# Kernel optimization log

Measured on AMD Instinct MI355X. Metric: run time of the kernel, lower is better.

The kernel has to match this reference:

```python
import math
import jax, jax.numpy as jnp
import numpy as np

BLOCK = 256
LAYER_IDX = 5
NUM_HIDDEN_LAYERS = 32


def get_slopes(head_dim):
    equ = lambda x: 1 / 2 ** (8 / x)
    log2 = math.log2(head_dim)
    if log2.is_integer():
        return [equ(head_dim) ** i for i in range(1, head_dim + 1)]
    lower = 2 ** math.floor(log2)
    upper = 2 ** math.ceil(log2)
    ls = get_slopes(lower)
    us = get_slopes(upper)
    return ls + us[::2][: head_dim - lower]


def setup_inputs() -> dict:
    key = jax.random.key(0)
    k1, k2, k3 = jax.random.split(key, 3)
    B, H, S, D = 2, 64, 4096, 64
    q = jax.random.normal(k1, (B, H, S, D), dtype=jnp.float32)
    k = jax.random.normal(k2, (B, H, S, D), dtype=jnp.float32)
    v = jax.random.normal(k3, (B, H, S, D), dtype=jnp.float32)
    mask = jnp.ones((B, S), dtype=jnp.int32)
    return {"query_states": q, "key_states": k, "value_states": v, "attention_mask": mask}


def _lightning_attention(q, k, v, attention_mask):
    B, H, S, D = q.shape
    E = v.shape[-1]
    # mask padded positions in values
    v = v * attention_mask[:, None, :, None].astype(v.dtype)

    # per-head decay slopes, scaled by layer depth (note: H == D by construction)
    slopes = np.asarray(get_slopes(D), dtype=np.float32)
    slopes = slopes * (1.0 - LAYER_IDX / (NUM_HIDDEN_LAYERS - 1) + 1e-05)
    slope = jnp.asarray(slopes)[:, None, None]  # [H, 1, 1]

    arr = jnp.arange(1, BLOCK + 1, dtype=jnp.float32)
    q_decay = jnp.exp(-slope * arr[:, None])            # [H, BLOCK, 1]
    k_decay = jnp.exp(-slope * (BLOCK - arr)[:, None])  # [H, BLOCK, 1]
    idx = arr[:, None] - arr[None, :]                   # [BLOCK, BLOCK]
    s_idx = slope * idx[None]                           # [H, BLOCK, BLOCK] (slope [H,1,1] broadcasts)
    diag_decay = jnp.exp(jnp.where(idx[None] >= 0, -s_idx, -jnp.inf))  # [H, BLOCK, BLOCK]
    block_decay = jnp.exp(-slope * BLOCK)               # [H, 1, 1]

    nb = S // BLOCK
    qb = q.reshape(B, H, nb, BLOCK, D).transpose(2, 0, 1, 3, 4)  # [nb, B, H, BLOCK, D]
    kb = k.reshape(B, H, nb, BLOCK, D).transpose(2, 0, 1, 3, 4)
    vb = v.reshape(B, H, nb, BLOCK, E).transpose(2, 0, 1, 3, 4)

    def step(kv, blk):
        qi, ki, vi = blk  # each [B, H, BLOCK, D/E]
        # inter-block: decayed query reads recurrent kv state
        o_inter = jnp.einsum('bhmd,bhde->bhme', qi * q_decay, kv)
        # intra-block: causal decayed attention within the block
        qk = jnp.einsum('bhmd,bhnd->bhmn', qi, ki) * diag_decay
        o_intra = jnp.einsum('bhmn,bhne->bhme', qk, vi)
        # update recurrent state
        kv_new = block_decay * kv + jnp.einsum('bhmd,bhme->bhde', ki * k_decay, vi)
        return kv_new, o_inter + o_intra

    kv0 = jnp.zeros((B, H, D, E), dtype=jnp.float32)
    _, outs = jax.lax.scan(step, kv0, (qb, kb, vb))  # outs: [nb, B, H, BLOCK, E]
    out = outs.transpose(1, 2, 0, 3, 4).reshape(B, H, S, E)
    return out


def reference(query_states, key_states, value_states, attention_mask):
    return _lightning_attention(query_states, key_states, value_states, attention_mask)
```

## Files before the change

### kernel.cpp

```cpp
#include <hip/hip_runtime.h>

typedef __attribute__((ext_vector_type(4))) float f4;
typedef __attribute__((ext_vector_type(4))) float f32x4;
typedef __attribute__((ext_vector_type(8))) short short8;
typedef __attribute__((ext_vector_type(4))) short short4v;

#define S_  4096
#define NB_ 16
#define SLOPE_SCALE 0.838719677419355f

__device__ __forceinline__ float slope_for_head(int h) {
    return exp2f(-(float)(h + 1) * 0.125f) * SLOPE_SCALE;
}

__device__ __forceinline__ short f2bf(float f) {
    unsigned u = __float_as_uint(f);
    u += 0x7FFFu + ((u >> 16) & 1u);
    return (short)(u >> 16);
}
__device__ __forceinline__ float bf2f(short s) {
    return __uint_as_float(((unsigned)(unsigned short)s) << 16);
}

template<int USE_KBF>
__global__ __launch_bounds__(256, 2) void phase1_kvblocks(
    const float* __restrict__ k, const float* __restrict__ v,
    const int* __restrict__ mask, float* __restrict__ kvt,
    short* __restrict__ vt, short* __restrict__ kbf)
{
    __shared__ float ks[64][64];
    __shared__ float vs[64][64];
    __shared__ short khi[64][72];
    __shared__ short klo[64][72];
    __shared__ short vhi[64][72];
    __shared__ short vlo[64][72];
    const int j  = blockIdx.x;
    const int bh = blockIdx.y;
    const int b  = bh >> 6;
    const int h  = bh & 63;
    const int t  = threadIdx.x;
    const int wave = t >> 6, lane = t & 63, quad = lane >> 4, l16 = lane & 15;
    const float slope = slope_for_head(h);

    const f32x4 zf = {0.f, 0.f, 0.f, 0.f};
    f32x4 acc[4];
    acc[0] = zf; acc[1] = zf; acc[2] = zf; acc[3] = zf;

    const long long tilebase = ((long long)bh * S_ + j * 256) * 64;
    const long long vtbase   = ((long long)(bh * NB_ + j)) * 16384;

    for (int c = 0; c < 4; ++c) {
        for (int i = 0; i < 4; ++i) {
            int fi  = t + i * 256;
            int row = fi >> 4;
            int col = (fi & 15) << 2;
            long long g = tilebase + (long long)(c * 64 + row) * 64 + col;
            f4 kk = *(const f4*)(k + g);
            if (USE_KBF) {
                short4v kb = { f2bf(kk.x), f2bf(kk.y), f2bf(kk.z), f2bf(kk.w) };
                *(short4v*)(kbf + g) = kb;
            }
            float kd = __expf(-slope * (float)(255 - (c * 64 + row)));
            *(f4*)&ks[row][col] = kk * kd;
            f4 vv = *(const f4*)(v + g);
            float mv = (float)mask[b * S_ + j * 256 + c * 64 + row];
            *(f4*)&vs[row][col] = vv * mv;
        }
        __syncthreads();

        {
            const int dl = lane;
            #pragma unroll
            for (int r = 0; r < 16; r += 8) {
                short8 k8h, k8l, v8h, v8l;
                #pragma unroll
                for (int rr = 0; rr < 8; ++rr) {
                    int n = wave * 16 + r + rr;
                    float kx = ks[n][dl];
                    short kh = f2bf(kx);
                    k8h[rr] = kh; k8l[rr] = f2bf(kx - bf2f(kh));
                    float vx = vs[n][dl];
                    short vh = f2bf(vx);
                    v8h[rr] = vh; v8l[rr] = f2bf(vx - bf2f(vh));
                }
                *(short8*)&khi[dl][wave * 16 + r] = k8h;
                *(short8*)&klo[dl][wave * 16 + r] = k8l;
                *(short8*)&vhi[dl][wave * 16 + r] = v8h;
                *(short8*)&vlo[dl][wave * 16 + r] = v8l;
            }
        }
        __syncthreads();

        {
            int e  = t >> 2;
            int nb = (t & 3) << 4;
            short8 w0 = *(const short8*)&vhi[e][nb];
            short8 w1 = *(const short8*)&vhi[e][nb + 8];
            long long g = vtbase + (long long)(c * 2 + (nb >> 5)) * 2048
                        + e * 32 + (nb & 31);
            *(short8*)(vt + g)     = w0;
            *(short8*)(vt + g + 8) = w1;
        }

        #pragma unroll
        for (int cc = 0; cc < 2; ++cc) {
            const int nb = cc * 32 + quad * 8;
            short8 ahi = *(const short8*)&vhi[wave * 16 + l16][nb];
            short8 alo = *(const short8*)&vlo[wave * 16 + l16][nb];
            #pragma unroll
            for (int dt = 0; dt < 4; ++dt) {
                short8 bhi = *(const short8*)&khi[dt * 16 + l16][nb];
                short8 blo = *(const short8*)&klo[dt * 16 + l16][nb];
                acc[dt] = __builtin_amdgcn_mfma_f32_16x16x32_bf16(ahi, bhi, acc[dt], 0, 0, 0);
                acc[dt] = __builtin_amdgcn_mfma_f32_16x16x32_bf16(ahi, blo, acc[dt], 0, 0, 0);
                acc[dt] = __builtin_amdgcn_mfma_f32_16x16x32_bf16(alo, bhi, acc[dt], 0, 0, 0);
            }
        }
        __syncthreads();
    }

    float* o = kvt + ((long long)(bh * NB_ + j)) * 4096;
    #pragma unroll
    for (int dt = 0; dt < 4; ++dt) {
        #pragma unroll
        for (int r = 0; r < 4; ++r) {
            int e = wave * 16 + quad * 4 + r;
            o[e * 64 + dt * 16 + l16] = acc[dt][r];
        }
    }
}

__global__ __launch_bounds__(256) void phase2_scan(float* __restrict__ kvt)
{
    const int g    = blockIdx.x;
    const int bh   = g >> 2;
    const int part = g & 3;
    const int h    = bh & 63;
    const float slope = slope_for_head(h);
    const float bd = __expf(-slope * 256.0f);

    f4* base = (f4*)(kvt + (long long)bh * NB_ * 4096) + part * 256 + threadIdx.x;
    f4 vals[NB_];
    #pragma unroll
    for (int jj = 0; jj < NB_; ++jj) vals[jj] = base[jj * 1024];
    f4 st = {0.f, 0.f, 0.f, 0.f};
    #pragma unroll
    for (int jj = 0; jj < NB_; ++jj) {
        base[jj * 1024] = st;
        st = st * bd + vals[jj];
    }
}

template<int USE_KBF>
__global__ __launch_bounds__(256, 2) void phase3_output(
    const float* __restrict__ q, const float* __restrict__ kfp,
    const short* __restrict__ kbf, const float* __restrict__ kvt,
    const short* __restrict__ vt, float* __restrict__ out)
{
    __shared__ short P[4][64 * 56];
    const int j    = blockIdx.x;
    const int bh   = blockIdx.y;
    const int h    = bh & 63;
    const int tid  = threadIdx.x;
    const int wave = tid >> 6;
    const int lane = tid & 63;
    const int quad = lane >> 4;
    const int l16  = lane & 15;
    const int wrole  = (wave + j) & 3;
    const float slope = slope_for_head(h);
    const int mwbase = wrole << 6;

    const long long rowbase = (long long)bh * S_ + j * 256 + mwbase;

    short8 qf[4][2];
    #pragma unroll
    for (int mt = 0; mt < 4; ++mt) {
        const float* qp = q + (rowbase + mt * 16 + l16) * 64 + quad * 8;
        #pragma unroll
        for (int ks = 0; ks < 2; ++ks) {
            f4 a = *(const f4*)(qp + ks * 32);
            f4 b = *(const f4*)(qp + ks * 32 + 4);
            short8 f;
            f[0] = f2bf(a.x); f[1] = f2bf(a.y); f[2] = f2bf(a.z); f[3] = f2bf(a.w);
            f[4] = f2bf(b.x); f[5] = f2bf(b.y); f[6] = f2bf(b.z); f[7] = f2bf(b.w);
            qf[mt][ks] = f;
        }
    }

    const f32x4 zf = {0.f, 0.f, 0.f, 0.f};
    f32x4 of[4][4];
    #pragma unroll
    for (int et = 0; et < 4; ++et)
        #pragma unroll
        for (int mt = 0; mt < 4; ++mt) of[et][mt] = zf;

    const float* kvp = kvt + ((long long)(bh * NB_ + j) << 12);
    #pragma unroll
    for (int et = 0; et < 4; ++et) {
        #pragma unroll
        for (int ks = 0; ks < 2; ++ks) {
            const float* p = kvp + (et * 16 + l16) * 64 + ks * 32 + quad * 8;
            f4 a = *(const f4*)(p);
            f4 b = *(const f4*)(p + 4);
            short8 af;
            af[0] = f2bf(a.x); af[1] = f2bf(a.y); af[2] = f2bf(a.z); af[3] = f2bf(a.w);
            af[4] = f2bf(b.x); af[5] = f2bf(b.y); af[6] = f2bf(b.z); af[7] = f2bf(b.w);
            #pragma unroll
            for (int mt = 0; mt < 4; ++mt)
                of[et][mt] = __builtin_amdgcn_mfma_f32_16x16x32_bf16(
                    af, qf[mt][ks], of[et][mt], 0, 0, 0);
        }
    }
    #pragma unroll
    for (int mt = 0; mt < 4; ++mt) {
        float qd = __expf(-slope * (float)(mwbase + mt * 16 + l16 + 1));
        #pragma unroll
        for (int et = 0; et < 4; ++et) of[et][mt] *= qd;
    }

    const float er1 = __expf(slope);
    const float er2 = er1 * er1;
    const float er3 = er2 * er1;
    short* Pw = &P[wave][0];
    const int nchunks = (mwbase >> 5) + 2;
    const long long kTile = ((long long)bh * S_ + j * 256) * 64;
    const long long vTile = ((long long)(bh * NB_ + j)) * 16384;

    for (int c = 0; c < nchunks; ++c) {
        const int nbase = c << 5;

        short8 kf[2][2];
        if (USE_KBF) {
            #pragma unroll
            for (int nt = 0; nt < 2; ++nt) {
                const short* kp = kbf + kTile
                    + (long long)(nbase + nt * 16 + l16) * 64 + quad * 8;
                kf[nt][0] = *(const short8*)(kp);
                kf[nt][1] = *(const short8*)(kp + 32);
            }
        } else {
            #pragma unroll
            for (int nt = 0; nt < 2; ++nt) {
                const float* kp = kfp + kTile
                    + (long long)(nbase + nt * 16 + l16) * 64 + quad * 8;
                #pragma unroll
                for (int ks = 0; ks < 2; ++ks) {
                    f4 a = *(const f4*)(kp + ks * 32);
                    f4 b = *(const f4*)(kp + ks * 32 + 4);
                    short8 f;
                    f[0] = f2bf(a.x); f[1] = f2bf(a.y); f[2] = f2bf(a.z); f[3] = f2bf(a.w);
                    f[4] = f2bf(b.x); f[5] = f2bf(b.y); f[6] = f2bf(b.z); f[7] = f2bf(b.w);
                    kf[nt][ks] = f;
                }
            }
        }

        f32x4 sf[2][4];
        #pragma unroll
        for (int nt = 0; nt < 2; ++nt)
            #pragma unroll
            for (int mt = 0; mt < 4; ++mt) sf[nt][mt] = zf;
        #pragma unroll
        for (int nt = 0; nt < 2; ++nt)
            #pragma unroll
            for (int ks = 0; ks < 2; ++ks)
                #pragma unroll
                for (int mt = 0; mt < 4; ++mt)
                    sf[nt][mt] = __builtin_amdgcn_mfma_f32_16x16x32_bf16(
                        kf[nt][ks], qf[mt][ks], sf[nt][mt], 0, 0, 0);

        #pragma unroll
        for (int nt = 0; nt < 2; ++nt) {
            #pragma unroll
            for (int mt = 0; mt < 4; ++mt) {
                int n0 = nbase + nt * 16 + quad * 4;
                int m  = mwbase + mt * 16 + l16;
                float ddb = __expf(-slope * (float)(m - n0));
                f32x4 s = sf[nt][mt];
                float v0 = (m >= n0)     ? s[0] * ddb       : 0.f;
                float v1 = (m >= n0 + 1) ? s[1] * ddb * er1 : 0.f;
                float v2 = (m >= n0 + 2) ? s[2] * ddb * er2 : 0.f;
                float v3 = (m >= n0 + 3) ? s[3] * ddb * er3 : 0.f;
                short4v pk = {f2bf(v0), f2bf(v1), f2bf(v2), f2bf(v3)};
                *(short4v*)&Pw[(mt * 16 + l16) * 56 + nt * 16 + quad * 4] = pk;
            }
        }
        asm volatile("s_waitcnt lgkmcnt(0)" ::: "memory");

        short8 pb[4];
        #pragma unroll
        for (int mt = 0; mt < 4; ++mt)
            pb[mt] = *(const short8*)&Pw[(mt * 16 + l16) * 56 + quad * 8];
        short8 va[4];
        #pragma unroll
        for (int et = 0; et < 4; ++et)
            va[et] = *(const short8*)(vt + vTile + c * 2048
                                      + (et * 16 + l16) * 32 + quad * 8);

        #pragma unroll
        for (int et = 0; et < 4; ++et)
            #pragma unroll
            for (int mt = 0; mt < 4; ++mt)
                of[et][mt] = __builtin_amdgcn_mfma_f32_16x16x32_bf16(
                    va[et], pb[mt], of[et][mt], 0, 0, 0);
    }

    #pragma unroll
    for (int mt = 0; mt < 4; ++mt) {
        float* orow = out + (rowbase + mt * 16 + l16) * 64;
        #pragma unroll
        for (int et = 0; et < 4; ++et) {
            f4 o = {of[et][mt][0], of[et][mt][1], of[et][mt][2], of[et][mt][3]};
            *(f4*)(orow + et * 16 + quad * 4) = o;
        }
    }
}

extern "C" void kernel_launch(void* const* d_in, const int* in_sizes, int n_in,
                              void* d_out, int out_size, void* d_ws, size_t ws_size,
                              hipStream_t stream) {
    const float* q    = (const float*)d_in[0];
    const float* k    = (const float*)d_in[1];
    const float* v    = (const float*)d_in[2];
    const int*   mask = (const int*)d_in[3];
    float* kvt = (float*)d_ws;
    short* vt  = (short*)((char*)d_ws + (size_t)33554432);
    short* kbf = (short*)((char*)d_ws + (size_t)33554432 + 67108864);
    float* out = (float*)d_out;

    const bool use_kbf = ws_size >= (size_t)167772160;
    if (use_kbf) {
        phase1_kvblocks<1><<<dim3(16, 128), 256, 0, stream>>>(k, v, mask, kvt, vt, kbf);
        phase2_scan<<<512, 256, 0, stream>>>(kvt);
        phase3_output<1><<<dim3(16, 128), 256, 0, stream>>>(q, k, kbf, kvt, vt, out);
    } else {
        phase1_kvblocks<0><<<dim3(16, 128), 256, 0, stream>>>(k, v, mask, kvt, vt, kbf);
        phase2_scan<<<512, 256, 0, stream>>>(kvt);
        phase3_output<0><<<dim3(16, 128), 256, 0, stream>>>(q, k, kbf, kvt, vt, out);
    }
}
```

Before: 518.3 us.

## Pipeline K/V staging, swizzle LDS, emit bf16 KV state, prefetch K chunks

Phase 1 now works in 32-row sub-tiles with register prefetch of the next K/V sub-tile, a smaller XOR-swizzled LDS layout, and higher occupancy bounds. Phase 2 can also write a bf16 copy of the scanned KV state, so phase 3 loads packed bf16 instead of converting fp32. Phase 3 double-buffers the bf16 K fragments across chunks, issues the V loads earlier, and replaces the per-element exp with precomputed decay factors. The bf16 state path only runs if the workspace is large enough, and the extra register buffers may add register pressure.

Measured after the change: 496.2 us. 4.3% less time.

```diff
diff --git a/kernel.cpp b/kernel.cpp
--- a/kernel.cpp
+++ b/kernel.cpp
@@ -22,18 +22,22 @@
     return __uint_as_float(((unsigned)(unsigned short)s) << 16);
 }
 
+__device__ __forceinline__ int NX(int row, int n8) {
+    return n8 ^ (((row >> 3) & 3) << 3);
+}
+
 template<int USE_KBF>
-__global__ __launch_bounds__(256, 2) void phase1_kvblocks(
+__global__ __launch_bounds__(256, 4) void phase1_kvblocks(
     const float* __restrict__ k, const float* __restrict__ v,
     const int* __restrict__ mask, float* __restrict__ kvt,
     short* __restrict__ vt, short* __restrict__ kbf)
 {
-    __shared__ float ks[64][64];
-    __shared__ float vs[64][64];
-    __shared__ short khi[64][72];
-    __shared__ short klo[64][72];
-    __shared__ short vhi[64][72];
-    __shared__ short vlo[64][72];
+    __shared__ float ks[32][64];
+    __shared__ float vs[32][64];
+    __shared__ short khi[64][40];
+    __shared__ short klo[64][40];
+    __shared__ short vhi[64][40];
+    __shared__ short vlo[64][40];
     const int j  = blockIdx.x;
     const int bh = blockIdx.y;
     const int b  = bh >> 6;
@@ -49,68 +53,77 @@
     const long long tilebase = ((long long)bh * S_ + j * 256) * 64;
     const long long vtbase   = ((long long)(bh * NB_ + j)) * 16384;
 
-    for (int c = 0; c < 4; ++c) {
-        for (int i = 0; i < 4; ++i) {
-            int fi  = t + i * 256;
-            int row = fi >> 4;
-            int col = (fi & 15) << 2;
-            long long g = tilebase + (long long)(c * 64 + row) * 64 + col;
-            f4 kk = *(const f4*)(k + g);
+    const int r0  = t >> 4;
+    const int col = (t & 15) << 2;
+
+    f4 kr0, kr1, vr0, vr1; int mr0, mr1;
+    auto LOADSTG = [&](int ss) {
+        long long g0 = tilebase + (long long)(ss * 32 + r0) * 64 + col;
+        kr0 = *(const f4*)(k + g0);
+        vr0 = *(const f4*)(v + g0);
+        kr1 = *(const f4*)(k + g0 + 16 * 64);
+        vr1 = *(const f4*)(v + g0 + 16 * 64);
+        mr0 = mask[b * S_ + j * 256 + ss * 32 + r0];
+        mr1 = mask[b * S_ + j * 256 + ss * 32 + r0 + 16];
+    };
+    LOADSTG(0);
+
+    for (int ss = 0; ss < 8; ++ss) {
+        {
+            int gn0 = ss * 32 + r0;
             if (USE_KBF) {
-                short4v kb = { f2bf(kk.x), f2bf(kk.y), f2bf(kk.z), f2bf(kk.w) };
-                *(short4v*)(kbf + g) = kb;
-            }
-            float kd = __expf(-slope * (float)(255 - (c * 64 + row)));
-            *(f4*)&ks[row][col] = kk * kd;
-            f4 vv = *(const f4*)(v + g);
-            float mv = (float)mask[b * S_ + j * 256 + c * 64 + row];
-            *(f4*)&vs[row][col] = vv * mv;
-        }
+                long long g0 = tilebase + (long long)gn0 * 64 + col;
+                short4v kb0 = { f2bf(kr0.x), f2bf(kr0.y), f2bf(kr0.z), f2bf(kr0.w) };
+                short4v kb1 = { f2bf(kr1.x), f2bf(kr1.y), f2bf(kr1.z), f2bf(kr1.w) };
+                *(short4v*)(kbf + g0)           = kb0;
+                *(short4v*)(kbf + g0 + 16 * 64) = kb1;
+            }
+            float kd0 = __expf(-slope * (float)(255 - gn0));
+            float kd1 = __expf(-slope * (float)(255 - gn0 - 16));
+            *(f4*)&ks[r0][col]      = kr0 * kd0;
+            *(f4*)&ks[r0 + 16][col] = kr1 * kd1;
+            *(f4*)&vs[r0][col]      = vr0 * (float)mr0;
+            *(f4*)&vs[r0 + 16][col] = vr1 * (float)mr1;
+        }
+        if (ss < 7) LOADSTG(ss + 1);
         __syncthreads();
 
         {
             const int dl = lane;
-            #pragma unroll
-            for (int r = 0; r < 16; r += 8) {
-                short8 k8h, k8l, v8h, v8l;
-                #pragma unroll
-                for (int rr = 0; rr < 8; ++rr) {
-                    int n = wave * 16 + r + rr;
-                    float kx = ks[n][dl];
-                    short kh = f2bf(kx);
-                    k8h[rr] = kh; k8l[rr] = f2bf(kx - bf2f(kh));
-                    float vx = vs[n][dl];
-                    short vh = f2bf(vx);
-                    v8h[rr] = vh; v8l[rr] = f2bf(vx - bf2f(vh));
-                }
-                *(short8*)&khi[dl][wave * 16 + r] = k8h;
-                *(short8*)&klo[dl][wave * 16 + r] = k8l;
-                *(short8*)&vhi[dl][wave * 16 + r] = v8h;
-                *(short8*)&vlo[dl][wave * 16 + r] = v8l;
-            }
+            short8 k8h, k8l, v8h, v8l;
+            #pragma unroll
+            for (int rr = 0; rr < 8; ++rr) {
+                float kx = ks[wave * 8 + rr][dl];
+                short kh = f2bf(kx);
+                k8h[rr] = kh; k8l[rr] = f2bf(kx - bf2f(kh));
+                float vx = vs[wave * 8 + rr][dl];
+                short vh = f2bf(vx);
+                v8h[rr] = vh; v8l[rr] = f2bf(vx - bf2f(vh));
+            }
+            int ni = NX(dl, wave * 8);
+            *(short8*)&khi[dl][ni] = k8h;
+            *(short8*)&klo[dl][ni] = k8l;
+            *(short8*)&vhi[dl][ni] = v8h;
+            *(short8*)&vlo[dl][ni] = v8l;
         }
         __syncthreads();
 
         {
             int e  = t >> 2;
-            int nb = (t & 3) << 4;
-            short8 w0 = *(const short8*)&vhi[e][nb];
-            short8 w1 = *(const short8*)&vhi[e][nb + 8];
-            long long g = vtbase + (long long)(c * 2 + (nb >> 5)) * 2048
-                        + e * 32 + (nb & 31);
-            *(short8*)(vt + g)     = w0;
-            *(short8*)(vt + g + 8) = w1;
-        }
-
-        #pragma unroll
-        for (int cc = 0; cc < 2; ++cc) {
-            const int nb = cc * 32 + quad * 8;
-            short8 ahi = *(const short8*)&vhi[wave * 16 + l16][nb];
-            short8 alo = *(const short8*)&vlo[wave * 16 + l16][nb];
+            int nb = (t & 3) << 3;
+            short8 w = *(const short8*)&vhi[e][NX(e, nb)];
+            *(short8*)(vt + vtbase + ss * 2048 + e * 32 + nb) = w;
+        }
+
+        {
+            int ar = wave * 16 + l16;
+            short8 ahi = *(const short8*)&vhi[ar][NX(ar, quad * 8)];
+            short8 alo = *(const short8*)&vlo[ar][NX(ar, quad * 8)];
             #pragma unroll
             for (int dt = 0; dt < 4; ++dt) {
-                short8 bhi = *(const short8*)&khi[dt * 16 + l16][nb];
-                short8 blo = *(const short8*)&klo[dt * 16 + l16][nb];
+                int br = dt * 16 + l16;
+                short8 bhi = *(const short8*)&khi[br][NX(br, quad * 8)];
+                short8 blo = *(const short8*)&klo[br][NX(br, quad * 8)];
                 acc[dt] = __builtin_amdgcn_mfma_f32_16x16x32_bf16(ahi, bhi, acc[dt], 0, 0, 0);
                 acc[dt] = __builtin_amdgcn_mfma_f32_16x16x32_bf16(ahi, blo, acc[dt], 0, 0, 0);
                 acc[dt] = __builtin_amdgcn_mfma_f32_16x16x32_bf16(alo, bhi, acc[dt], 0, 0, 0);
@@ -130,7 +143,9 @@
     }
 }
 
-__global__ __launch_bounds__(256) void phase2_scan(float* __restrict__ kvt)
+template<int EMIT>
+__global__ __launch_bounds__(256) void phase2_scan(float* __restrict__ kvt,
+                                                   short* __restrict__ kvb)
 {
     const int g    = blockIdx.x;
     const int bh   = g >> 2;
@@ -140,6 +155,8 @@
     const float bd = __expf(-slope * 256.0f);
 
     f4* base = (f4*)(kvt + (long long)bh * NB_ * 4096) + part * 256 + threadIdx.x;
+    short* kb = kvb + (long long)bh * NB_ * 4096
+              + ((long long)(part * 256 + threadIdx.x) << 2);
     f4 vals[NB_];
     #pragma unroll
     for (int jj = 0; jj < NB_; ++jj) vals[jj] = base[jj * 1024];
@@ -147,15 +164,20 @@
     #pragma unroll
     for (int jj = 0; jj < NB_; ++jj) {
         base[jj * 1024] = st;
+        if (EMIT) {
+            short4v sb = { f2bf(st.x), f2bf(st.y), f2bf(st.z), f2bf(st.w) };
+            *(short4v*)(kb + (long long)jj * 4096) = sb;
+        }
         st = st * bd + vals[jj];
     }
 }
 
-template<int USE_KBF>
-__global__ __launch_bounds__(256, 2) void phase3_output(
+template<int USE_KBF, int USE_KVB>
+__global__ __launch_bounds__(256, 3) void phase3_output(
     const float* __restrict__ q, const float* __restrict__ kfp,
     const short* __restrict__ kbf, const float* __restrict__ kvt,
-    const short* __restrict__ vt, float* __restrict__ out)
+    const short* __restrict__ kvb, const short* __restrict__ vt,
+    float* __restrict__ out)
 {
     __shared__ short P[4][64 * 56];
     const int j    = blockIdx.x;
@@ -171,6 +193,8 @@
     const int mwbase = wrole << 6;
 
     const long long rowbase = (long long)bh * S_ + j * 256 + mwbase;
+    const long long kTile = ((long long)bh * S_ + j * 256) * 64;
+    const long long vTile = ((long long)(bh * NB_ + j)) * 16384;
 
     short8 qf[4][2];
     #pragma unroll
@@ -187,6 +211,19 @@
         }
     }
 
+    auto LOADKF = [&](short8 (&dst)[2][2], int nb0) {
+        #pragma unroll
+        for (int nt = 0; nt < 2; ++nt) {
+            const short* kp = kbf + kTile
+                + (long long)(nb0 + nt * 16 + l16) * 64 + quad * 8;
+            dst[nt][0] = *(const short8*)(kp);
+            dst[nt][1] = *(const short8*)(kp + 32);
+        }
+    };
+
+    short8 kfA[2][2];
+    if (USE_KBF) LOADKF(kfA, 0);
+
     const f32x4 zf = {0.f, 0.f, 0.f, 0.f};
     f32x4 of[4][4];
     #pragma unroll
@@ -194,21 +231,37 @@
         #pragma unroll
         for (int mt = 0; mt < 4; ++mt) of[et][mt] = zf;
 
-    const float* kvp = kvt + ((long long)(bh * NB_ + j) << 12);
-    #pragma unroll
-    for (int et = 0; et < 4; ++et) {
-        #pragma unroll
-        for (int ks = 0; ks < 2; ++ks) {
-            const float* p = kvp + (et * 16 + l16) * 64 + ks * 32 + quad * 8;
-            f4 a = *(const f4*)(p);
-            f4 b = *(const f4*)(p + 4);
-            short8 af;
-            af[0] = f2bf(a.x); af[1] = f2bf(a.y); af[2] = f2bf(a.z); af[3] = f2bf(a.w);
-            af[4] = f2bf(b.x); af[5] = f2bf(b.y); af[6] = f2bf(b.z); af[7] = f2bf(b.w);
-            #pragma unroll
-            for (int mt = 0; mt < 4; ++mt)
-                of[et][mt] = __builtin_amdgcn_mfma_f32_16x16x32_bf16(
-                    af, qf[mt][ks], of[et][mt], 0, 0, 0);
+    if (USE_KVB) {
+        const short* kvbp = kvb + ((long long)(bh * NB_ + j) << 12);
+        #pragma unroll
+        for (int et = 0; et < 4; ++et) {
+            #pragma unroll
+            for (int ks = 0; ks < 2; ++ks) {
+                short8 af = *(const short8*)(kvbp + (et * 16 + l16) * 64
+                                             + ks * 32 + quad * 8);
+                #pragma unroll
+                for (int mt = 0; mt < 4; ++mt)
+                    of[et][mt] = __builtin_amdgcn_mfma_f32_16x16x32_bf16(
+                        af, qf[mt][ks], of[et][mt], 0, 0, 0);
+            }
+        }
+    } else {
+        const float* kvp = kvt + ((long long)(bh * NB_ + j) << 12);
+        #pragma unroll
+        for (int et = 0; et < 4; ++et) {
+            #pragma unroll
+            for (int ks = 0; ks < 2; ++ks) {
+                const float* p = kvp + (et * 16 + l16) * 64 + ks * 32 + quad * 8;
+                f4 a = *(const f4*)(p);
+                f4 b = *(const f4*)(p + 4);
+                short8 af;
+                af[0] = f2bf(a.x); af[1] = f2bf(a.y); af[2] = f2bf(a.z); af[3] = f2bf(a.w);
+                af[4] = f2bf(b.x); af[5] = f2bf(b.y); af[6] = f2bf(b.z); af[7] = f2bf(b.w);
+                #pragma unroll
+                for (int mt = 0; mt < 4; ++mt)
+                    of[et][mt] = __builtin_amdgcn_mfma_f32_16x16x32_bf16(
+                        af, qf[mt][ks], of[et][mt], 0, 0, 0);
+            }
         }
     }
     #pragma unroll
@@ -221,24 +274,28 @@
     const float er1 = __expf(slope);
     const float er2 = er1 * er1;
     const float er3 = er2 * er1;
+    const float L  = __expf(-slope * (float)(l16 - quad * 4));
+    const float T1 = __expf(-slope * 16.f);
+    const float Ti = __expf(slope * 16.f);
+    const float Tm[4] = {1.f, T1, T1 * T1, T1 * T1 * T1};
+
     short* Pw = &P[wave][0];
     const int nchunks = (mwbase >> 5) + 2;
-    const long long kTile = ((long long)bh * S_ + j * 256) * 64;
-    const long long vTile = ((long long)(bh * NB_ + j)) * 16384;
 
     for (int c = 0; c < nchunks; ++c) {
         const int nbase = c << 5;
-
-        short8 kf[2][2];
-        if (USE_KBF) {
-            #pragma unroll
-            for (int nt = 0; nt < 2; ++nt) {
-                const short* kp = kbf + kTile
-                    + (long long)(nbase + nt * 16 + l16) * 64 + quad * 8;
-                kf[nt][0] = *(const short8*)(kp);
-                kf[nt][1] = *(const short8*)(kp + 32);
-            }
-        } else {
+        const bool havenext = (c + 1 < nchunks);
+
+        short8 va[4];
+        #pragma unroll
+        for (int et = 0; et < 4; ++et)
+            va[et] = *(const short8*)(vt + vTile + c * 2048
+                                      + (et * 16 + l16) * 32 + quad * 8);
+
+        short8 kfB[2][2];
+        if (USE_KBF && havenext) LOADKF(kfB, nbase + 32);
+
+        if (!USE_KBF) {
             #pragma unroll
             for (int nt = 0; nt < 2; ++nt) {
                 const float* kp = kfp + kTile
@@ -250,7 +307,7 @@
                     short8 f;
                     f[0] = f2bf(a.x); f[1] = f2bf(a.y); f[2] = f2bf(a.z); f[3] = f2bf(a.w);
                     f[4] = f2bf(b.x); f[5] = f2bf(b.y); f[6] = f2bf(b.z); f[7] = f2bf(b.w);
-                    kf[nt][ks] = f;
+                    kfA[nt][ks] = f;
                 }
             }
         }
@@ -267,15 +324,17 @@
                 #pragma unroll
                 for (int mt = 0; mt < 4; ++mt)
                     sf[nt][mt] = __builtin_amdgcn_mfma_f32_16x16x32_bf16(
-                        kf[nt][ks], qf[mt][ks], sf[nt][mt], 0, 0, 0);
-
+                        kfA[nt][ks], qf[mt][ks], sf[nt][mt], 0, 0, 0);
+
+        const float WL = __expf(-slope * (float)(mwbase - nbase)) * L;
         #pragma unroll
         for (int nt = 0; nt < 2; ++nt) {
             #pragma unroll
             for (int mt = 0; mt < 4; ++mt) {
                 int n0 = nbase + nt * 16 + quad * 4;
                 int m  = mwbase + mt * 16 + l16;
-                float ddb = __expf(-slope * (float)(m - n0));
+                float ddb = WL * Tm[mt];
+                if (nt) ddb *= Ti;
                 f32x4 s = sf[nt][mt];
                 float v0 = (m >= n0)     ? s[0] * ddb       : 0.f;
                 float v1 = (m >= n0 + 1) ? s[1] * ddb * er1 : 0.f;
@@ -291,11 +350,6 @@
         #pragma unroll
         for (int mt = 0; mt < 4; ++mt)
             pb[mt] = *(const short8*)&Pw[(mt * 16 + l16) * 56 + quad * 8];
-        short8 va[4];
-        #pragma unroll
-        for (int et = 0; et < 4; ++et)
-            va[et] = *(const short8*)(vt + vTile + c * 2048
-                                      + (et * 16 + l16) * 32 + quad * 8);
 
         #pragma unroll
         for (int et = 0; et < 4; ++et)
@@ -303,6 +357,14 @@
             for (int mt = 0; mt < 4; ++mt)
                 of[et][mt] = __builtin_amdgcn_mfma_f32_16x16x32_bf16(
                     va[et], pb[mt], of[et][mt], 0, 0, 0);
+
+        if (USE_KBF && havenext) {
+            #pragma unroll
+            for (int nt = 0; nt < 2; ++nt) {
+                kfA[nt][0] = kfB[nt][0];
+                kfA[nt][1] = kfB[nt][1];
+            }
+        }
     }
 
     #pragma unroll
@@ -325,17 +387,21 @@
     const int*   mask = (const int*)d_in[3];
     float* kvt = (float*)d_ws;
     short* vt  = (short*)((char*)d_ws + (size_t)33554432);
-    short* kbf = (short*)((char*)d_ws + (size_t)33554432 + 67108864);
+    short* kbf = (short*)((char*)d_ws + (size_t)100663296);
+    short* kvb = (short*)((char*)d_ws + (size_t)167772160);
     float* out = (float*)d_out;
 
-    const bool use_kbf = ws_size >= (size_t)167772160;
-    if (use_kbf) {
+    if (ws_size >= (size_t)184549376) {
         phase1_kvblocks<1><<<dim3(16, 128), 256, 0, stream>>>(k, v, mask, kvt, vt, kbf);
-        phase2_scan<<<512, 256, 0, stream>>>(kvt);
-        phase3_output<1><<<dim3(16, 128), 256, 0, stream>>>(q, k, kbf, kvt, vt, out);
+        phase2_scan<1><<<512, 256, 0, stream>>>(kvt, kvb);
+        phase3_output<1, 1><<<dim3(16, 128), 256, 0, stream>>>(q, k, kbf, kvt, kvb, vt, out);
+    } else if (ws_size >= (size_t)167772160) {
+        phase1_kvblocks<1><<<dim3(16, 128), 256, 0, stream>>>(k, v, mask, kvt, vt, kbf);
+        phase2_scan<0><<<512, 256, 0, stream>>>(kvt, kvb);
+        phase3_output<1, 0><<<dim3(16, 128), 256, 0, stream>>>(q, k, kbf, kvt, kvb, vt, out);
     } else {
         phase1_kvblocks<0><<<dim3(16, 128), 256, 0, stream>>>(k, v, mask, kvt, vt, kbf);
-        phase2_scan<<<512, 256, 0, stream>>>(kvt);
-        phase3_output<0><<<dim3(16, 128), 256, 0, stream>>>(q, k, kbf, kvt, vt, out);
-    }
-}
+        phase2_scan<0><<<512, 256, 0, stream>>>(kvt, kvb);
+        phase3_output<0, 0><<<dim3(16, 128), 256, 0, stream>>>(q, k, kbf, kvt, kvb, vt, out);
+    }
+}
```
